# Optimization experiments

Hardware: AMD Instinct MI355X
Metric: run time of the kernel (lower is better)

Reference implementation:

```python
import jax, jax.numpy as jnp
import numpy as np

TOD, DOW = 288, 7
INPUT_LEN, OUTPUT_LEN = 12, 12
N_NODES, R_PATCH, LAYERS = 883, 8, 3
D_IN, D_NODE, D_TOD, D_DOW = 64, 32, 32, 32
DIMS = D_IN + D_NODE + D_TOD + D_DOW  # 160
HID = 2 * DIMS
NEG = -1e9  # finite large-negative mask (avoids NaN on fully-masked rows)


def setup_inputs():
    key = jax.random.key(0)
    ks = jax.random.split(key, 16)
    B = 8
    x = jax.random.normal(ks[0], (B, INPUT_LEN, N_NODES, 1), jnp.float32)
    te = jax.random.randint(ks[1], (B, INPUT_LEN, N_NODES, 2), 0, 7, dtype=jnp.int32)
    s = 0.1
    return {
        "x": x,
        "te": te,
        "patch_emb": jax.random.normal(ks[2], (R_PATCH, D_NODE), jnp.float32) * s,
        "node_table": jax.random.normal(ks[3], (N_NODES, D_NODE), jnp.float32) * s,
        "tod_emb": jax.random.normal(ks[4], (TOD, D_TOD), jnp.float32) * s,
        "dow_emb": jax.random.normal(ks[5], (DOW, D_DOW), jnp.float32) * s,
        "conv_W": jax.random.normal(ks[6], (D_IN, 3, INPUT_LEN), jnp.float32) * s,
        "conv_b": jnp.zeros((D_IN,), jnp.float32),
        # 4 layernorms per layer: [iro1, iro2, ier1, ier2]
        "ln_scale": jnp.ones((LAYERS, 4, DIMS), jnp.float32),
        "ln_bias": jnp.zeros((LAYERS, 4, DIMS), jnp.float32),
        # attn: axis1 = [iro, ier]; axis2 = [q, k, v, out], weights stored [in, out]
        "attn_W": jax.random.normal(ks[7], (LAYERS, 2, 4, DIMS, DIMS), jnp.float32) * 0.05,
        "attn_b": jnp.zeros((LAYERS, 2, 4, DIMS), jnp.float32),
        "mlp_W1": jax.random.normal(ks[8], (LAYERS, 2, DIMS, HID), jnp.float32) * 0.05,
        "mlp_b1": jnp.zeros((LAYERS, 2, HID), jnp.float32),
        "mlp_W2": jax.random.normal(ks[9], (LAYERS, 2, HID, DIMS), jnp.float32) * 0.05,
        "mlp_b2": jnp.zeros((LAYERS, 2, DIMS), jnp.float32),
        "out_W": jax.random.normal(ks[10], (OUTPUT_LEN, DIMS), jnp.float32) * 0.05,
        "out_b": jnp.zeros((OUTPUT_LEN,), jnp.float32),
    }


def _layernorm(x, g, b):
    mu = jnp.mean(x, axis=-1, keepdims=True)
    var = jnp.mean(jnp.square(x - mu), axis=-1, keepdims=True)
    return (x - mu) / jnp.sqrt(var + 1e-5) * g + b


def _mha(x, W, b, key_mask):
    # single-head attention (num_heads=1 in PatchID); x: [..., S, D]
    q = x @ W[0] + b[0]
    k = x @ W[1] + b[1]
    v = x @ W[2] + b[2]
    score = jnp.einsum('...sd,...td->...st', q, k) / np.sqrt(x.shape[-1]).astype(np.float32)
    score = jnp.where(key_mask[..., None, :], score, NEG)
    w = jax.nn.softmax(score, axis=-1)
    o = jnp.einsum('...st,...td->...sd', w, v)
    return o @ W[3] + b[3]


def _forward(x, te, patch_emb, node_table, tod_emb, dow_emb, conv_W, conv_b,
             ln_scale, ln_bias, attn_W, attn_b, mlp_W1, mlp_b1, mlp_W2, mlp_b2,
             out_W, out_b):
    N, R = N_NODES, R_PATCH
    # ---- PatchClassifier (router) ----
    logits = node_table @ patch_emb.T                       # [N, R]
    probs = jax.nn.softmax(logits, axis=-1)
    patch_ids = jnp.argmax(probs, axis=-1)                  # [N]
    hard = jax.nn.one_hot(patch_ids, R, dtype=probs.dtype)
    probs_st = hard - jax.lax.stop_gradient(probs) + probs  # straight-through
    node_soft = probs @ patch_emb                           # [N, D_NODE]
    # ---- embedding ----
    B, T_in = x.shape[0], x.shape[1]
    T = T_in // INPUT_LEN  # = 1
    tef = te.astype(x.dtype)
    x1 = jnp.concatenate([x, tef[..., 0:1] / TOD, tef[..., 1:2] / DOW], axis=-1)  # [B,T_in,N,3]
    x1 = x1.reshape(B, T, INPUT_LEN, N, 3)
    feat = jnp.einsum('btlnc,dcl->btnd', x1, conv_W) + conv_b  # patchified conv
    tid = te[:, -T:, :, 0]
    diw = te[:, -T:, :, 1]
    emb = jnp.concatenate([
        feat, tod_emb[tid], dow_emb[diw],
        jnp.broadcast_to(node_soft, (B, T, N, D_NODE)),
    ], axis=-1)                                             # [B,T,N,DIMS]
    # ---- group_by_patch (static P = N upper bound, masked) ----
    onehot = patch_ids[:, None] == jnp.arange(R)[None, :]
    pos = jnp.cumsum(onehot.astype(jnp.int32), axis=0)[jnp.arange(N), patch_ids] - 1
    P = N
    pf = jnp.zeros((B, T, R, P, DIMS), emb.dtype).at[:, :, patch_ids, pos, :].set(emb)
    mask2d = jnp.zeros((R, P), bool).at[patch_ids, pos].set(True)
    km_iro = mask2d[None, None]       # [1,1,R,P] valid-key mask, keys = P axis
    km_ier = mask2d.T[None, None]     # [1,1,P,R] valid-key mask, keys = R axis
    # ---- encoder layers ----
    for l in range(LAYERS):
        # intra-patch attention over P
        xn = _layernorm(pf, ln_scale[l, 0], ln_bias[l, 0])
        pf = pf + _mha(xn, attn_W[l, 0], attn_b[l, 0], km_iro)
        h = _layernorm(pf, ln_scale[l, 1], ln_bias[l, 1])
        pf = pf + (jax.nn.gelu(h @ mlp_W1[l, 0] + mlp_b1[l, 0], approximate=False)
                   @ mlp_W2[l, 0] + mlp_b2[l, 0])
        # inter-patch attention over R
        xt = jnp.swapaxes(pf, 2, 3)  # [B,T,P,R,D]
        xn = _layernorm(xt, ln_scale[l, 2], ln_bias[l, 2])
        xt = xt + _mha(xn, attn_W[l, 1], attn_b[l, 1], km_ier)
        pf = jnp.swapaxes(xt, 2, 3)
        h = _layernorm(pf, ln_scale[l, 3], ln_bias[l, 3])
        pf = pf + (jax.nn.gelu(h @ mlp_W1[l, 1] + mlp_b1[l, 1], approximate=False)
                   @ mlp_W2[l, 1] + mlp_b2[l, 1])
    # ---- ungroup + 1x1 output conv ----
    out_feat = pf[:, :, patch_ids, pos, :]                  # [B,T,N,DIMS]
    pred = jnp.einsum('btnd,od->bont', out_feat, out_W) + out_b[None, :, None, None]
    return pred, probs_st


def reference(x, te, patch_emb, node_table, tod_emb, dow_emb, conv_W, conv_b,
              ln_scale, ln_bias, attn_W, attn_b, mlp_W1, mlp_b1, mlp_W2, mlp_b2,
              out_W, out_b):
    return _forward(x, te, patch_emb, node_table, tod_emb, dow_emb, conv_W, conv_b,
                    ln_scale, ln_bias, attn_W, attn_b, mlp_W1, mlp_b1, mlp_W2,
                    mlp_b2, out_W, out_b)
```

## Files before the change

kernel.cpp:

```cpp
#include <hip/hip_runtime.h>
#include <math.h>

#define NNODES 883
#define BB 8
#define DIMS_ 160
#define HID_ 320
#define PBB 1008
#define RMAX2 (BB*PBB)
#define RMAXP (RMAX2+64)
#define GXNUM (RMAX2/16)

typedef __attribute__((ext_vector_type(8))) short short8v;
typedef __attribute__((ext_vector_type(4))) float fx4;
typedef __attribute__((ext_vector_type(4))) unsigned short ushort4v;

__device__ __forceinline__ unsigned short f2bf(float f) {
  unsigned int u = __float_as_uint(f);
  u = (u + 0x7fffu + ((u >> 16) & 1u)) >> 16;
  return (unsigned short)u;
}
__device__ __forceinline__ float bf2f(unsigned short u) {
  return __uint_as_float(((unsigned int)u) << 16);
}
__device__ __forceinline__ float gelu_f(float v) {
  return 0.5f*v*(1.f + erff(v*0.70710678118654752f));
}

__global__ __launch_bounds__(256)
void zero_pf(float4* __restrict__ p, int n4) {
  int i = blockIdx.x*256 + threadIdx.x;
  if (i < n4) p[i] = float4{0.f, 0.f, 0.f, 0.f};
}

__global__ __launch_bounds__(128)
void patch_kernel(const float* __restrict__ node_table,
                  const float* __restrict__ patch_emb,
                  float* __restrict__ probs_st,
                  float* __restrict__ nsoft,
                  int* __restrict__ patch_ids) {
  int n = blockIdx.x * blockDim.x + threadIdx.x;
  if (n >= NNODES) return;
  float nt[32];
#pragma unroll
  for (int j = 0; j < 32; ++j) nt[j] = node_table[n*32 + j];
  float lg[8];
#pragma unroll
  for (int r = 0; r < 8; ++r) {
    float a = 0.f;
#pragma unroll
    for (int j = 0; j < 32; ++j) a += nt[j] * patch_emb[r*32 + j];
    lg[r] = a;
  }
  float m = lg[0];
#pragma unroll
  for (int r = 1; r < 8; ++r) m = fmaxf(m, lg[r]);
  float e[8]; float s = 0.f;
#pragma unroll
  for (int r = 0; r < 8; ++r) { e[r] = expf(lg[r] - m); s += e[r]; }
  float p[8];
#pragma unroll
  for (int r = 0; r < 8; ++r) p[r] = e[r] / s;
  int am = 0; float best = p[0];
#pragma unroll
  for (int r = 1; r < 8; ++r) if (p[r] > best) { best = p[r]; am = r; }
  patch_ids[n] = am;
#pragma unroll
  for (int r = 0; r < 8; ++r) {
    float hard = (r == am) ? 1.f : 0.f;
    probs_st[n*8 + r] = (hard - p[r]) + p[r];
  }
#pragma unroll
  for (int j = 0; j < 32; ++j) {
    float a = 0.f;
#pragma unroll
    for (int r = 0; r < 8; ++r) a += p[r] * patch_emb[r*32 + j];
    nsoft[n*32 + j] = a;
  }
}

__global__ __launch_bounds__(1024)
void scan_kernel(const int* __restrict__ patch_ids,
                 int* __restrict__ pk, int* __restrict__ cnt,
                 int* __restrict__ offs, int* __restrict__ cntmax) {
  __shared__ int pid_s[NNODES];
  __shared__ int cnt_s[8], offs_s[8];
  int t = threadIdx.x;
  if (t < 8) cnt_s[t] = 0;
  for (int n = t; n < NNODES; n += 1024) pid_s[n] = patch_ids[n];
  __syncthreads();
  int p = -1, pos = 0;
  if (t < NNODES) {
    p = pid_s[t];
    atomicAdd(&cnt_s[p], 1);
    for (int m = 0; m < t; ++m) pos += (pid_s[m] == p) ? 1 : 0;
  }
  __syncthreads();
  if (t == 0) {
    int o = 0, mx = 0;
#pragma unroll
    for (int r = 0; r < 8; ++r) {
      offs_s[r] = o; offs[r] = o; cnt[r] = cnt_s[r];
      if (cnt_s[r] > mx) mx = cnt_s[r];
      o += (cnt_s[r] + 15) & ~15;
    }
    cntmax[0] = mx;
  }
  __syncthreads();
  if (t < NNODES) pk[t] = offs_s[p] + pos;
}

__global__ __launch_bounds__(160)
void embed_kernel(const float* __restrict__ x, const int* __restrict__ te,
                  const float* __restrict__ convW, const float* __restrict__ convB,
                  const float* __restrict__ tod, const float* __restrict__ dow,
                  const float* __restrict__ nsoft, const int* __restrict__ pk,
                  const float* __restrict__ g, const float* __restrict__ bt,
                  float* __restrict__ pf, unsigned short* __restrict__ xn) {
  int n = blockIdx.x, b = blockIdx.y, t = threadIdx.x;
  __shared__ float xs[3][12];
  __shared__ float rsum[160], rss[160];
  __shared__ float musv[2];
  if (t < 12) {
    int l = t;
    xs[0][l] = x[(b*12 + l)*NNODES + n];
    int base = ((b*12 + l)*NNODES + n)*2;
    xs[1][l] = (float)te[base]     / 288.0f;
    xs[2][l] = (float)te[base + 1] / 7.0f;
  }
  __syncthreads();
  int row = b*PBB + pk[n];
  float val;
  if (t < 64) {
    float a = convB[t];
#pragma unroll
    for (int c = 0; c < 3; ++c)
#pragma unroll
      for (int l = 0; l < 12; ++l)
        a += xs[c][l] * convW[t*36 + c*12 + l];
    val = a;
  } else if (t < 96) {
    int ti = te[((b*12 + 11)*NNODES + n)*2 + 0];
    val = tod[ti*32 + (t - 64)];
  } else if (t < 128) {
    int dw = te[((b*12 + 11)*NNODES + n)*2 + 1];
    val = dow[dw*32 + (t - 96)];
  } else {
    val = nsoft[n*32 + (t - 128)];
  }
  pf[row*DIMS_ + t] = val;
  rsum[t] = val; rss[t] = val*val;
  __syncthreads();
  if (t < 32) {
    float s = 0.f, ss = 0.f;
#pragma unroll
    for (int j = 0; j < 5; ++j) { s += rsum[t + 32*j]; ss += rss[t + 32*j]; }
    s  += __shfl_xor(s, 1, 32);  ss += __shfl_xor(ss, 1, 32);
    s  += __shfl_xor(s, 2, 32);  ss += __shfl_xor(ss, 2, 32);
    s  += __shfl_xor(s, 4, 32);  ss += __shfl_xor(ss, 4, 32);
    s  += __shfl_xor(s, 8, 32);  ss += __shfl_xor(ss, 8, 32);
    s  += __shfl_xor(s, 16, 32); ss += __shfl_xor(ss, 16, 32);
    if (t == 0) {
      float mu = s*(1.f/160.f);
      float var = ss*(1.f/160.f) - mu*mu;
      musv[0] = mu; musv[1] = rsqrtf(var + 1e-5f);
    }
  }
  __syncthreads();
  xn[(size_t)row*DIMS_ + t] = f2bf((val - musv[0])*musv[1]*g[t] + bt[t]);
}

__global__ __launch_bounds__(256)
void cvt_all(const float* __restrict__ attn_W, const float* __restrict__ mlp_W1,
             const float* __restrict__ mlp_W2,
             unsigned short* __restrict__ wt_attn, unsigned short* __restrict__ wt_w1,
             unsigned short* __restrict__ wt_w2) {
  int y = blockIdx.y;
  const float* src; unsigned short* dst; int K, N;
  if (y < 24)      { src = attn_W + (size_t)y*25600;        dst = wt_attn + (size_t)y*25600; K = 160; N = 160; }
  else if (y < 30) { int q = y-24; src = mlp_W1 + (size_t)q*160*320; dst = wt_w1 + (size_t)q*51200; K = 160; N = 320; }
  else             { int q = y-30; src = mlp_W2 + (size_t)q*320*160; dst = wt_w2 + (size_t)q*51200; K = 320; N = 160; }
  int tn = N >> 5, tk = K >> 5;
  int tile = blockIdx.x;
  if (tile >= tn*tk) return;
  int n0 = (tile % tn) << 5, k0 = (tile / tn) << 5;
  __shared__ unsigned short lds[32][33];
  int col = threadIdx.x & 31, rb = threadIdx.x >> 5;
#pragma unroll
  for (int rr = 0; rr < 4; ++rr) {
    int row = rb + 8*rr;
    lds[row][col] = f2bf(src[(size_t)(k0 + row)*N + n0 + col]);
  }
  __syncthreads();
#pragma unroll
  for (int rr = 0; rr < 4; ++rr) {
    int row = rb + 8*rr;
    dst[(size_t)(n0 + row)*K + k0 + col] = lds[col][row];
  }
}

template<int K, bool TRANSV, int CT>
__global__ __launch_bounds__(64)
void mfma_mm(const unsigned short* __restrict__ Xv, const unsigned short* __restrict__ Wt,
             const float* __restrict__ bias, unsigned short* __restrict__ Cv,
             int M, int Cstride, size_t Wystep, size_t Cystep, int bystep) {
  constexpr int NS = K / 32;
  int lane = threadIdx.x;
  int r15  = lane & 15;
  int kg   = lane >> 4;
  int row0 = blockIdx.x * 16;
  int colbase = blockIdx.y * (CT*16);
  int z = blockIdx.z;
  Wt   += (size_t)z * Wystep;
  bias += (size_t)z * bystep;

  int ar = row0 + r15; if (ar > M-1) ar = M-1;
  short8v afrag[NS];
  const unsigned short* Xr = Xv + (size_t)ar*K + kg*8;
#pragma unroll
  for (int t = 0; t < NS; ++t)
    afrag[t] = *(const short8v*)(const void*)(Xr + t*32);

  fx4 acc[CT];
#pragma unroll
  for (int n = 0; n < CT; ++n) acc[n] = (fx4){0.f,0.f,0.f,0.f};

  const unsigned short* Wb = Wt + (size_t)(colbase + r15)*K + kg*8;
#pragma unroll
  for (int t = 0; t < NS; ++t)
#pragma unroll
    for (int n = 0; n < CT; ++n) {
      short8v bfr = *(const short8v*)(const void*)(Wb + (size_t)n*16*K + t*32);
      acc[n] = __builtin_amdgcn_mfma_f32_16x16x32_bf16(afrag[t], bfr, acc[n], 0, 0, 0);
    }

  int orow0 = row0 + kg*4;
  unsigned short* C = Cv + (size_t)z * Cystep;
#pragma unroll
  for (int n = 0; n < CT; ++n) {
    int col = colbase + n*16 + r15;
    float bv = bias[col];
#pragma unroll
    for (int i = 0; i < 4; ++i) {
      int rr = orow0 + i;
      if (rr >= M) continue;
      unsigned short h = f2bf(acc[n][i] + bv);
      if (TRANSV && z == 2) C[(size_t)col*RMAXP + rr] = h;
      else                  C[(size_t)rr*Cstride + col] = h;
    }
  }
}

template<bool INTRA, bool HASNEXT, bool TRANSV_NEXT>
__global__ __launch_bounds__(512)
void fused_layer(const unsigned short* __restrict__ qb,
                 const unsigned short* __restrict__ kb,
                 const unsigned short* __restrict__ vt,
                 const unsigned short* __restrict__ wproj, const float* __restrict__ bproj,
                 const unsigned short* __restrict__ w1, const float* __restrict__ b1v,
                 const unsigned short* __restrict__ w2, const float* __restrict__ b2v,
                 const float* __restrict__ g1, const float* __restrict__ bt1,
                 const float* __restrict__ gn, const float* __restrict__ btn,
                 const unsigned short* __restrict__ wqkvN, const float* __restrict__ bqkvN,
                 float* __restrict__ pf, unsigned short* __restrict__ qbN, size_t CY,
                 const int* __restrict__ cnt, const int* __restrict__ offs) {
  __shared__ unsigned short L1s[16*192];
  __shared__ unsigned short L2s[16*320];
  __shared__ float sA[8][16], ssA[8][16];
  __shared__ float Sf[INTRA ? 16*256 : 1];
  __shared__ unsigned short Pl[INTRA ? 16*256 : 1];
  __shared__ float Sinv[16];
  __shared__ int cs[8], os[8];
  char* L1 = (char*)L1s; char* L2 = (char*)L2s; char* Pb = (char*)Pl;
  const float scale = 0.07905694150420949f;

  int tid = threadIdx.x;
  int wid = tid >> 6;
  int lane = tid & 63;
  int r15 = lane & 15, kg = lane >> 4;
  int row0 = blockIdx.x * 16;
  if (tid < 8) { cs[tid] = cnt[tid]; os[tid] = offs[tid]; }
  __syncthreads();
  int b = row0 / PBB;
  int local = row0 - b*PBB;
  int r = 7;
#pragma unroll
  for (int rr = 6; rr >= 0; --rr) if (local < os[rr+1]) r = rr;
  int L = cs[r];
  int q0 = local - os[r];
  int bo = b*PBB + os[r];
  int ntP = (wid < 2) ? 2 : 1;
  int ntM = (wid < 4) ? 3 : 2;

  if (INTRA) {
    int nkt = (L + 15) >> 4;
    int npv = (L + 31) >> 5;
    short8v qf[5];
    {
      const unsigned short* Qr = qb + (size_t)(row0 + r15)*DIMS_ + kg*8;
#pragma unroll
      for (int kk = 0; kk < 5; ++kk) qf[kk] = *(const short8v*)(const void*)(Qr + kk*32);
    }
#pragma unroll
    for (int u = 0; u < 2; ++u) {
      int t = wid + 8*u;
      if (t < nkt) {
        fx4 a = (fx4){0.f,0.f,0.f,0.f};
        const unsigned short* Kr = kb + (size_t)(bo + t*16 + r15)*DIMS_ + kg*8;
#pragma unroll
        for (int kk = 0; kk < 5; ++kk) {
          short8v kf = *(const short8v*)(const void*)(Kr + kk*32);
          a = __builtin_amdgcn_mfma_f32_16x16x32_bf16(qf[kk], kf, a, 0, 0, 0);
        }
        int j = t*16 + r15;
#pragma unroll
        for (int i = 0; i < 4; ++i)
          Sf[(4*kg + i)*256 + j] = (j < L) ? a[i]*scale : -1e30f;
// ... 247 lines not shown
#pragma unroll
  for (int u = 0; u < 2; ++u)
    if (u < ntP) {
      int n = wid + 8*u;
      int col = n*16 + r15;
      float bv = b2v[col];
#pragma unroll
      for (int i = 0; i < 4; ++i) {
        float v = pn[u][i] + acc3[u][i] + bv;
        fnv[u][i] = v;
        pf[(size_t)(row0 + 4*kg + i)*DIMS_ + col] = v;
        sv2[i] += v; ssv2[i] += v*v;
      }
    }
  if (!HASNEXT) return;

#pragma unroll
  for (int i = 0; i < 4; ++i) {
    sv2[i] += __shfl_xor(sv2[i], 1, 16); ssv2[i] += __shfl_xor(ssv2[i], 1, 16);
    sv2[i] += __shfl_xor(sv2[i], 2, 16); ssv2[i] += __shfl_xor(ssv2[i], 2, 16);
    sv2[i] += __shfl_xor(sv2[i], 4, 16); ssv2[i] += __shfl_xor(ssv2[i], 4, 16);
    sv2[i] += __shfl_xor(sv2[i], 8, 16); ssv2[i] += __shfl_xor(ssv2[i], 8, 16);
  }
  __syncthreads();
  if (r15 == 0) {
#pragma unroll
    for (int i = 0; i < 4; ++i) { sA[wid][4*kg+i] = sv2[i]; ssA[wid][4*kg+i] = ssv2[i]; }
  }
  __syncthreads();
#pragma unroll
  for (int i = 0; i < 4; ++i) {
    float st = 0.f, sst = 0.f;
#pragma unroll
    for (int w = 0; w < 8; ++w) { st += sA[w][4*kg+i]; sst += ssA[w][4*kg+i]; }
    mu[i] = st*(1.f/160.f);
    float var = sst*(1.f/160.f) - mu[i]*mu[i];
    rs[i] = rsqrtf(var + 1e-5f);
  }
#pragma unroll
  for (int u = 0; u < 2; ++u)
    if (u < ntP) {
      int n = wid + 8*u;
      int col = n*16 + r15;
      float gv = gn[col], bv = btn[col];
#pragma unroll
      for (int i = 0; i < 4; ++i) {
        int row = 4*kg + i;
        int byte = row*384 + ((col*2) ^ ((row & 7) << 4));
        *(unsigned short*)(L1 + byte) = f2bf((fnv[u][i] - mu[i])*rs[i]*gv + bv);
      }
    }
  __syncthreads();

  fx4 accq[4];
#pragma unroll
  for (int u = 0; u < 4; ++u) accq[u] = (fx4){0.f,0.f,0.f,0.f};
#pragma unroll
  for (int t = 0; t < 5; ++t) {
    short8v a4 = *(const short8v*)(const void*)(L1 + r15*384 + ((t*64 + kg*16) ^ ((r15 & 7) << 4)));
#pragma unroll
    for (int u = 0; u < 4; ++u) {
      int n = wid + 8*u;
      if (n < 30) {
        int z = n / 10, nn = n - z*10;
        short8v bfr = *(const short8v*)(const void*)
            (wqkvN + (size_t)z*25600 + (size_t)(nn*16 + r15)*160 + t*32 + kg*8);
        accq[u] = __builtin_amdgcn_mfma_f32_16x16x32_bf16(a4, bfr, accq[u], 0, 0, 0);
      }
    }
  }
#pragma unroll
  for (int u = 0; u < 4; ++u) {
    int n = wid + 8*u;
    if (n >= 30) continue;
    int z = n / 10, nn = n - z*10;
    int col = nn*16 + r15;
    float bv = bqkvN[z*160 + col];
    unsigned short* C = qbN + (size_t)z * CY;
#pragma unroll
    for (int i = 0; i < 4; ++i) {
      int rr = row0 + 4*kg + i;
      unsigned short h = f2bf(accq[u][i] + bv);
      if (TRANSV_NEXT && z == 2) C[(size_t)col*RMAXP + rr] = h;
      else                       C[(size_t)rr*DIMS_ + col] = h;
    }
  }
}

__global__ __launch_bounds__(256)
void out_kernel(const float* __restrict__ pf, const float* __restrict__ outW,
                const float* __restrict__ outB, const int* __restrict__ pk,
                float* __restrict__ out) {
  int idx = blockIdx.x*256 + threadIdx.x;
  if (idx >= BB*12*NNODES) return;
  int n = idx % NNODES;
  int rest = idx / NNODES;
  int o = rest % 12;
  int b = rest / 12;
  int row = b*PBB + pk[n];
  const float4* Pr = (const float4*)&pf[(size_t)row*DIMS_];
  const float4* Wr = (const float4*)&outW[o*DIMS_];
  float ax=0.f, ay=0.f, az=0.f, aw=0.f;
#pragma unroll
  for (int d4 = 0; d4 < 40; ++d4) {
    float4 a = Pr[d4], c = Wr[d4];
    ax += a.x*c.x; ay += a.y*c.y; az += a.z*c.z; aw += a.w*c.w;
  }
  out[idx] = (ax+ay+az+aw) + outB[o];
}

extern "C" void kernel_launch(void* const* d_in, const int* in_sizes, int n_in,
                              void* d_out, int out_size, void* d_ws, size_t ws_size,
                              hipStream_t stream) {
  const float* x         = (const float*)d_in[0];
  const int*   te        = (const int*)d_in[1];
  const float* patch_emb = (const float*)d_in[2];
  const float* node_tab  = (const float*)d_in[3];
  const float* tod_emb   = (const float*)d_in[4];
  const float* dow_emb   = (const float*)d_in[5];
  const float* conv_W    = (const float*)d_in[6];
  const float* conv_b    = (const float*)d_in[7];
  const float* ln_scale  = (const float*)d_in[8];
  const float* ln_bias   = (const float*)d_in[9];
  const float* attn_W    = (const float*)d_in[10];
  const float* attn_b    = (const float*)d_in[11];
  const float* mlp_W1    = (const float*)d_in[12];
  const float* mlp_b1    = (const float*)d_in[13];
  const float* mlp_W2    = (const float*)d_in[14];
  const float* mlp_b2    = (const float*)d_in[15];
  const float* out_W     = (const float*)d_in[16];
  const float* out_b     = (const float*)d_in[17];

  float* out = (float*)d_out;
  float* probs_st = out + BB*12*NNODES;

  const size_t CY = (size_t)(RMAX2 + 16) * DIMS_;

  char* W = (char*)d_ws;
  float* pf = (float*)W;                        W += (size_t)(RMAX2 + 16)*DIMS_*4;
  unsigned short* xn = (unsigned short*)W;      W += (size_t)(RMAX2 + 16)*DIMS_*2;
  unsigned short* qb = (unsigned short*)W;      W += CY*2;
  unsigned short* kb = (unsigned short*)W;      W += CY*2;
  unsigned short* vt = (unsigned short*)W;      W += (size_t)DIMS_*RMAXP*2;
  unsigned short* wt_attn = (unsigned short*)W; W += (size_t)24*160*160*2;
  unsigned short* wt_w1   = (unsigned short*)W; W += (size_t)6*320*160*2;
  unsigned short* wt_w2   = (unsigned short*)W; W += (size_t)6*160*320*2;
  float* nsoft = (float*)W;                     W += (size_t)NNODES*32*4;
  int* patch_ids = (int*)W;
  int* pk     = patch_ids + NNODES;
  int* cnt    = pk + NNODES;
  int* offs   = cnt + 8;
  int* cntmax = offs + 8;
  (void)vt;

  {
    int n4 = (RMAX2 + 16) * DIMS_ / 4;
    zero_pf<<<(n4 + 255)/256, 256, 0, stream>>>((float4*)pf, n4);
  }

  cvt_all<<<dim3(50, 36), 256, 0, stream>>>(attn_W, mlp_W1, mlp_W2, wt_attn, wt_w1, wt_w2);

  patch_kernel<<<(NNODES + 127)/128, 128, 0, stream>>>(node_tab, patch_emb, probs_st, nsoft, patch_ids);
  scan_kernel<<<1, 1024, 0, stream>>>(patch_ids, pk, cnt, offs, cntmax);
  embed_kernel<<<dim3(NNODES, BB), 160, 0, stream>>>(x, te, conv_W, conv_b, tod_emb, dow_emb,
                                                     nsoft, pk, ln_scale, ln_bias, pf, xn);

  mfma_mm<160,true,5><<<dim3(GXNUM,2,3), 64, 0, stream>>>(
      xn, wt_attn, attn_b, qb, RMAX2, DIMS_, 25600, CY, DIMS_);

  for (int l = 0; l < 3; ++l) {
    for (int a = 0; a < 2; ++a) {
      int wb = l*2 + a;
      const float* bbase = attn_b + (size_t)wb*4*DIMS_;
      const unsigned short* wqkv = wt_attn + (size_t)wb*4*25600;
      const float* g1  = ln_scale + (size_t)(l*4 + a*2 + 1)*DIMS_;
      const float* bt1 = ln_bias  + (size_t)(l*4 + a*2 + 1)*DIMS_;
      bool hasnext = !(l == 2 && a == 1);
      int nidx = (a == 0) ? (l*4 + 2) : ((l+1)*4);
      const float* gn  = hasnext ? ln_scale + (size_t)nidx*DIMS_ : nullptr;
      const float* btn = hasnext ? ln_bias  + (size_t)nidx*DIMS_ : nullptr;
      const unsigned short* wqkvN = hasnext ? wt_attn + (size_t)(wb+1)*4*25600 : nullptr;
      const float* bqkvN = hasnext ? attn_b + (size_t)(wb+1)*4*DIMS_ : nullptr;

      const unsigned short* wproj = wqkv + 3*25600;
      const float* bproj = bbase + 3*DIMS_;
      const unsigned short* w1 = wt_w1 + (size_t)wb*51200;
      const unsigned short* w2 = wt_w2 + (size_t)wb*51200;
      const float* b1v = mlp_b1 + (size_t)wb*HID_;
      const float* b2v = mlp_b2 + (size_t)wb*DIMS_;

      if (a == 0) {
        fused_layer<true,true,false><<<GXNUM, 512, 0, stream>>>(
            qb, qb + CY, qb + 2*CY, wproj, bproj, w1, b1v, w2, b2v,
            g1, bt1, gn, btn, wqkvN, bqkvN, pf, qb, CY, cnt, offs);
      } else if (hasnext) {
        fused_layer<false,true,true><<<GXNUM, 512, 0, stream>>>(
            qb, qb + CY, qb + 2*CY, wproj, bproj, w1, b1v, w2, b2v,
            g1, bt1, gn, btn, wqkvN, bqkvN, pf, qb, CY, cnt, offs);
      } else {
        fused_layer<false,false,false><<<GXNUM, 512, 0, stream>>>(
            qb, qb + CY, qb + 2*CY, wproj, bproj, w1, b1v, w2, b2v,
            g1, bt1, nullptr, nullptr, nullptr, nullptr, pf, qb, CY, cnt, offs);
      }
    }
  }

  out_kernel<<<(BB*12*NNODES + 255)/256, 256, 0, stream>>>(pf, out_W, out_b, pk, out);
}
```

Before: 276.8 us.

## Fuse all transformer layers into one cooperative kernel with grid syncs

```diff
diff --git a/kernel.cpp b/kernel.cpp
--- a/kernel.cpp
+++ b/kernel.cpp
@@ -1,5 +1,8 @@
 #include <hip/hip_runtime.h>
+#include <hip/hip_cooperative_groups.h>
 #include <math.h>
+
+namespace cg = cooperative_groups;
 
 #define NNODES 883
 #define BB 8
@@ -32,81 +35,75 @@
   if (i < n4) p[i] = float4{0.f, 0.f, 0.f, 0.f};
 }
 
-__global__ __launch_bounds__(128)
-void patch_kernel(const float* __restrict__ node_table,
-                  const float* __restrict__ patch_emb,
-                  float* __restrict__ probs_st,
-                  float* __restrict__ nsoft,
-                  int* __restrict__ patch_ids) {
-  int n = blockIdx.x * blockDim.x + threadIdx.x;
-  if (n >= NNODES) return;
-  float nt[32];
-#pragma unroll
-  for (int j = 0; j < 32; ++j) nt[j] = node_table[n*32 + j];
-  float lg[8];
-#pragma unroll
-  for (int r = 0; r < 8; ++r) {
-    float a = 0.f;
-#pragma unroll
-    for (int j = 0; j < 32; ++j) a += nt[j] * patch_emb[r*32 + j];
-    lg[r] = a;
-  }
-  float m = lg[0];
-#pragma unroll
-  for (int r = 1; r < 8; ++r) m = fmaxf(m, lg[r]);
-  float e[8]; float s = 0.f;
-#pragma unroll
-  for (int r = 0; r < 8; ++r) { e[r] = expf(lg[r] - m); s += e[r]; }
-  float p[8];
-#pragma unroll
-  for (int r = 0; r < 8; ++r) p[r] = e[r] / s;
-  int am = 0; float best = p[0];
-#pragma unroll
-  for (int r = 1; r < 8; ++r) if (p[r] > best) { best = p[r]; am = r; }
-  patch_ids[n] = am;
-#pragma unroll
-  for (int r = 0; r < 8; ++r) {
-    float hard = (r == am) ? 1.f : 0.f;
-    probs_st[n*8 + r] = (hard - p[r]) + p[r];
-  }
-#pragma unroll
-  for (int j = 0; j < 32; ++j) {
-    float a = 0.f;
-#pragma unroll
-    for (int r = 0; r < 8; ++r) a += p[r] * patch_emb[r*32 + j];
-    nsoft[n*32 + j] = a;
-  }
-}
-
 __global__ __launch_bounds__(1024)
-void scan_kernel(const int* __restrict__ patch_ids,
-                 int* __restrict__ pk, int* __restrict__ cnt,
-                 int* __restrict__ offs, int* __restrict__ cntmax) {
+void patch_scan(const float* __restrict__ node_table,
+                const float* __restrict__ patch_emb,
+                float* __restrict__ probs_st,
+                float* __restrict__ nsoft,
+                int* __restrict__ pk, int* __restrict__ cnt,
+                int* __restrict__ offs) {
+  __shared__ float pe[256];
   __shared__ int pid_s[NNODES];
   __shared__ int cnt_s[8], offs_s[8];
   int t = threadIdx.x;
+  for (int k = t; k < 256; k += 1024) pe[k] = patch_emb[k];
   if (t < 8) cnt_s[t] = 0;
-  for (int n = t; n < NNODES; n += 1024) pid_s[n] = patch_ids[n];
-  __syncthreads();
-  int p = -1, pos = 0;
+  __syncthreads();
+  int am = -1;
   if (t < NNODES) {
-    p = pid_s[t];
-    atomicAdd(&cnt_s[p], 1);
-    for (int m = 0; m < t; ++m) pos += (pid_s[m] == p) ? 1 : 0;
+    float nt[32];
+#pragma unroll
+    for (int j = 0; j < 32; ++j) nt[j] = node_table[t*32 + j];
+    float lg[8];
+#pragma unroll
+    for (int r = 0; r < 8; ++r) {
+      float a = 0.f;
+#pragma unroll
+      for (int j = 0; j < 32; ++j) a += nt[j] * pe[r*32 + j];
+      lg[r] = a;
+    }
+    float m = lg[0];
+#pragma unroll
+    for (int r = 1; r < 8; ++r) m = fmaxf(m, lg[r]);
+    float e[8]; float s = 0.f;
+#pragma unroll
+    for (int r = 0; r < 8; ++r) { e[r] = expf(lg[r] - m); s += e[r]; }
+    float p[8];
+#pragma unroll
+    for (int r = 0; r < 8; ++r) p[r] = e[r] / s;
+    am = 0; float best = p[0];
+#pragma unroll
+    for (int r = 1; r < 8; ++r) if (p[r] > best) { best = p[r]; am = r; }
+    pid_s[t] = am;
+    atomicAdd(&cnt_s[am], 1);
+#pragma unroll
+    for (int r = 0; r < 8; ++r) {
+      float hard = (r == am) ? 1.f : 0.f;
+      probs_st[t*8 + r] = (hard - p[r]) + p[r];
+    }
+#pragma unroll
+    for (int j = 0; j < 32; ++j) {
+      float a = 0.f;
+#pragma unroll
+      for (int r = 0; r < 8; ++r) a += p[r] * pe[r*32 + j];
+      nsoft[t*32 + j] = a;
+    }
   }
   __syncthreads();
   if (t == 0) {
-    int o = 0, mx = 0;
+    int o = 0;
 #pragma unroll
     for (int r = 0; r < 8; ++r) {
       offs_s[r] = o; offs[r] = o; cnt[r] = cnt_s[r];
-      if (cnt_s[r] > mx) mx = cnt_s[r];
       o += (cnt_s[r] + 15) & ~15;
     }
-    cntmax[0] = mx;
-  }
-  __syncthreads();
-  if (t < NNODES) pk[t] = offs_s[p] + pos;
+  }
+  __syncthreads();
+  if (t < NNODES) {
+    int pos = 0;
+    for (int m = 0; m < t; ++m) pos += (pid_s[m] == am) ? 1 : 0;
+    pk[t] = offs_s[am] + pos;
+  }
 }
 
 __global__ __launch_bounds__(160)
@@ -198,54 +195,446 @@
   }
 }
 
-template<int K, bool TRANSV, int CT>
-__global__ __launch_bounds__(64)
-void mfma_mm(const unsigned short* __restrict__ Xv, const unsigned short* __restrict__ Wt,
-             const float* __restrict__ bias, unsigned short* __restrict__ Cv,
-             int M, int Cstride, size_t Wystep, size_t Cystep, int bystep) {
-  constexpr int NS = K / 32;
-  int lane = threadIdx.x;
-  int r15  = lane & 15;
-  int kg   = lane >> 4;
+__device__ __forceinline__ void qkv_from_L1(const char* L1,
+    const unsigned short* __restrict__ wq, const float* __restrict__ bq,
+    unsigned short* __restrict__ qbN, bool transv,
+    int row0, int wid, int r15, int kg) {
+  constexpr size_t CY = (size_t)(RMAX2 + 16) * DIMS_;
+  fx4 accq[4];
+#pragma unroll
+  for (int u = 0; u < 4; ++u) accq[u] = (fx4){0.f,0.f,0.f,0.f};
+#pragma unroll
+  for (int t = 0; t < 5; ++t) {
+    short8v a4 = *(const short8v*)(const void*)(L1 + r15*384 + ((t*64 + kg*16) ^ ((r15 & 7) << 4)));
+#pragma unroll
+    for (int u = 0; u < 4; ++u) {
+      int n = wid + 8*u;
+      if (n < 30) {
+        int z = n / 10, nn = n - z*10;
+        short8v bfr = *(const short8v*)(const void*)
+            (wq + (size_t)z*25600 + (size_t)(nn*16 + r15)*160 + t*32 + kg*8);
+        accq[u] = __builtin_amdgcn_mfma_f32_16x16x32_bf16(a4, bfr, accq[u], 0, 0, 0);
+      }
+    }
+  }
+#pragma unroll
+  for (int u = 0; u < 4; ++u) {
+    int n = wid + 8*u;
+    if (n >= 30) continue;
+    int z = n / 10, nn = n - z*10;
+    int col = nn*16 + r15;
+    float bv = bq[z*160 + col];
+    unsigned short* C = qbN + (size_t)z * CY;
+#pragma unroll
+    for (int i = 0; i < 4; ++i) {
+      int rr = row0 + 4*kg + i;
+      unsigned short h = f2bf(accq[u][i] + bv);
+      if (transv && z == 2) C[(size_t)col*RMAXP + rr] = h;
+      else                  C[(size_t)rr*DIMS_ + col] = h;
+    }
+  }
+}
+
+__global__ __launch_bounds__(512, 4)
+void layers_coop(unsigned short* __restrict__ qbA, unsigned short* __restrict__ qbB,
+                 const unsigned short* __restrict__ wt_attn,
+                 const unsigned short* __restrict__ wt_w1,
+                 const unsigned short* __restrict__ wt_w2,
+                 const float* __restrict__ attn_b, const float* __restrict__ mlp_b1,
+                 const float* __restrict__ mlp_b2,
+                 const float* __restrict__ ln_scale, const float* __restrict__ ln_bias,
+                 const unsigned short* __restrict__ xn, float* __restrict__ pf,
+                 const int* __restrict__ cnt, const int* __restrict__ offs) {
+  constexpr size_t CY = (size_t)(RMAX2 + 16) * DIMS_;
+  cg::grid_group gg = cg::this_grid();
+  __shared__ unsigned short L1s[16*192];
+  __shared__ unsigned short L2s[16*320];
+  __shared__ float sA[8][16], ssA[8][16];
+  __shared__ float Sf[16*256];
+  __shared__ unsigned short Pl[16*256];
+  __shared__ float Sinv[16];
+  __shared__ int cs[8], os[8];
+  char* L1 = (char*)L1s; char* L2 = (char*)L2s; char* Pb = (char*)Pl;
+  const float scale = 0.07905694150420949f;
+
+  int tid = threadIdx.x;
+  int wid = tid >> 6;
+  int lane = tid & 63;
+  int r15 = lane & 15, kg = lane >> 4;
   int row0 = blockIdx.x * 16;
-  int colbase = blockIdx.y * (CT*16);
-  int z = blockIdx.z;
-  Wt   += (size_t)z * Wystep;
-  bias += (size_t)z * bystep;
-
-  int ar = row0 + r15; if (ar > M-1) ar = M-1;
-  short8v afrag[NS];
-  const unsigned short* Xr = Xv + (size_t)ar*K + kg*8;
-#pragma unroll
-  for (int t = 0; t < NS; ++t)
-    afrag[t] = *(const short8v*)(const void*)(Xr + t*32);
-
-  fx4 acc[CT];
-#pragma unroll
-  for (int n = 0; n < CT; ++n) acc[n] = (fx4){0.f,0.f,0.f,0.f};
-
-  const unsigned short* Wb = Wt + (size_t)(colbase + r15)*K + kg*8;
-#pragma unroll
-  for (int t = 0; t < NS; ++t)
-#pragma unroll
-    for (int n = 0; n < CT; ++n) {
-      short8v bfr = *(const short8v*)(const void*)(Wb + (size_t)n*16*K + t*32);
-      acc[n] = __builtin_amdgcn_mfma_f32_16x16x32_bf16(afrag[t], bfr, acc[n], 0, 0, 0);
-    }
-
-  int orow0 = row0 + kg*4;
-  unsigned short* C = Cv + (size_t)z * Cystep;
-#pragma unroll
-  for (int n = 0; n < CT; ++n) {
-    int col = colbase + n*16 + r15;
-    float bv = bias[col];
+  if (tid < 8) { cs[tid] = cnt[tid]; os[tid] = offs[tid]; }
+  __syncthreads();
+  int b = row0 / PBB;
+  int local = row0 - b*PBB;
+  int r = 7;
+#pragma unroll
+  for (int rr = 6; rr >= 0; --rr) if (local < os[rr+1]) r = rr;
+  int L = cs[r];
+  int q0 = local - os[r];
+  int bo = b*PBB + os[r];
+  int ntP = (wid < 2) ? 2 : 1;
+  int ntM = (wid < 4) ? 3 : 2;
+
+  for (int k = tid; k < 16*DIMS_; k += 512) {
+    int row = k / DIMS_, col = k - row*DIMS_;
+    int byte = row*384 + ((col*2) ^ ((row & 7) << 4));
+    *(unsigned short*)(L1 + byte) = xn[(size_t)(row0 + row)*DIMS_ + col];
+  }
+  __syncthreads();
+  qkv_from_L1(L1, wt_attn, attn_b, qbA, true, row0, wid, r15, kg);
+  __threadfence();
+  gg.sync();
+
+  for (int wb = 0; wb < 6; ++wb) {
+    bool intra = ((wb & 1) == 0);
+    bool hasnext = (wb < 5);
+    unsigned short* qbCur = (wb & 1) ? qbB : qbA;
+    unsigned short* qbNext = (wb & 1) ? qbA : qbB;
+    const unsigned short* qb = qbCur;
+    const unsigned short* kb = qbCur + CY;
+    const unsigned short* vt = qbCur + 2*CY;
+    const unsigned short* wqkv = wt_attn + (size_t)wb*4*25600;
+    const float* bbase = attn_b + (size_t)wb*4*DIMS_;
+    const unsigned short* wproj = wqkv + 3*25600;
+    const float* bproj = bbase + 3*DIMS_;
+    const unsigned short* w1 = wt_w1 + (size_t)wb*51200;
+    const unsigned short* w2 = wt_w2 + (size_t)wb*51200;
+    const float* b1v = mlp_b1 + (size_t)wb*HID_;
+    const float* b2v = mlp_b2 + (size_t)wb*DIMS_;
+    const float* g1  = ln_scale + (size_t)(2*wb + 1)*DIMS_;
+    const float* bt1 = ln_bias  + (size_t)(2*wb + 1)*DIMS_;
+    const float* gn  = ln_scale + (size_t)(2*wb + 2)*DIMS_;
+    const float* btn = ln_bias  + (size_t)(2*wb + 2)*DIMS_;
+    const unsigned short* wqkvN = wt_attn + (size_t)(wb+1)*4*25600;
+    const float* bqkvN = attn_b + (size_t)(wb+1)*4*DIMS_;
+
+    if (intra) {
+      int nkt = (L + 15) >> 4;
+      int npv = (L + 31) >> 5;
+      short8v qf[5];
+      {
+        const unsigned short* Qr = qb + (size_t)(row0 + r15)*DIMS_ + kg*8;
+#pragma unroll
+        for (int kk = 0; kk < 5; ++kk) qf[kk] = *(const short8v*)(const void*)(Qr + kk*32);
+      }
+#pragma unroll
+      for (int u = 0; u < 2; ++u) {
+        int t = wid + 8*u;
+        if (t < nkt) {
+          fx4 a = (fx4){0.f,0.f,0.f,0.f};
+          const unsigned short* Kr = kb + (size_t)(bo + t*16 + r15)*DIMS_ + kg*8;
+#pragma unroll
+          for (int kk = 0; kk < 5; ++kk) {
+            short8v kf = *(const short8v*)(const void*)(Kr + kk*32);
+            a = __builtin_amdgcn_mfma_f32_16x16x32_bf16(qf[kk], kf, a, 0, 0, 0);
+          }
+          int j = t*16 + r15;
+#pragma unroll
+          for (int i = 0; i < 4; ++i)
+            Sf[(4*kg + i)*256 + j] = (j < L) ? a[i]*scale : -1e30f;
+        }
+      }
+      __syncthreads();
+      {
+        int qq = lane >> 5, l32 = lane & 31;
+        int row = 2*wid + qq;
+        float vals[8];
+        float mx = -1e30f;
+#pragma unroll
+        for (int k = 0; k < 8; ++k) {
+          int j = l32 + 32*k;
+          float v = (j < L) ? Sf[row*256 + j] : -1e30f;
+          vals[k] = v; mx = fmaxf(mx, v);
+        }
+        mx = fmaxf(mx, __shfl_xor(mx, 1, 32));
+        mx = fmaxf(mx, __shfl_xor(mx, 2, 32));
+        mx = fmaxf(mx, __shfl_xor(mx, 4, 32));
+        mx = fmaxf(mx, __shfl_xor(mx, 8, 32));
+        mx = fmaxf(mx, __shfl_xor(mx, 16, 32));
+        float sum = 0.f;
+#pragma unroll
+        for (int k = 0; k < 8; ++k) {
+          float e = (vals[k] > -1e29f) ? expf(vals[k] - mx) : 0.f;
+          vals[k] = e; sum += e;
+        }
+        sum += __shfl_xor(sum, 1, 32);
+        sum += __shfl_xor(sum, 2, 32);
+        sum += __shfl_xor(sum, 4, 32);
+        sum += __shfl_xor(sum, 8, 32);
+        sum += __shfl_xor(sum, 16, 32);
+        if (l32 == 0) Sinv[row] = (sum > 0.f) ? 1.f/sum : 0.f;
+#pragma unroll
+        for (int k = 0; k < 8; ++k) {
+          int j = l32 + 32*k;
+          int byte = row*512 + ((j*2) ^ ((row & 7) << 4));
+          *(unsigned short*)(Pb + byte) = f2bf(vals[k]);
+        }
+      }
+      __syncthreads();
+      fx4 o[2];
+#pragma unroll
+      for (int u = 0; u < 2; ++u) o[u] = (fx4){0.f,0.f,0.f,0.f};
+#pragma unroll
+      for (int sS = 0; sS < 8; ++sS) {
+        if (sS < npv) {
+          short8v pfr = *(const short8v*)(const void*)
+              (Pb + r15*512 + ((sS*64 + kg*16) ^ ((r15 & 7) << 4)));
+#pragma unroll
+          for (int u = 0; u < 2; ++u)
+            if (u < ntP) {
+              int n = wid + 8*u;
+              const unsigned short* Vr = vt + (size_t)(n*16 + r15)*RMAXP + bo + sS*32 + kg*8;
+              short8v vf = *(const short8v*)(const void*)Vr;
+              o[u] = __builtin_amdgcn_mfma_f32_16x16x32_bf16(pfr, vf, o[u], 0, 0, 0);
+            }
+        }
+      }
+      float inv[4];
+#pragma unroll
+      for (int i = 0; i < 4; ++i) inv[i] = Sinv[4*kg + i];
+#pragma unroll
+      for (int u = 0; u < 2; ++u)
+        if (u < ntP) {
+          int n = wid + 8*u;
+#pragma unroll
+          for (int i = 0; i < 4; ++i) {
+            int row = 4*kg + i, d = n*16 + r15;
+            int byte = row*384 + ((d*2) ^ ((row & 7) << 4));
+            *(unsigned short*)(L1 + byte) = f2bf(o[u][i]*inv[i]);
+          }
+        }
+    } else {
+      int qq = lane >> 5, l32 = lane & 31;
+      int rowT = 2*wid + qq;
+      int p = q0 + rowT;
+      bool vq = p < L;
+      int j = l32 >> 2, c = l32 & 3;
+      int cj = cs[j];
+      bool vk = p < cj;
+      int keyrow = b*PBB + os[j] + (vk ? p : 0);
+      int qrow = row0 + rowT;
+      float part = 0.f;
+      {
+        const unsigned short* qr = qb + (size_t)qrow*DIMS_ + c*40;
+        const unsigned short* kr = kb + (size_t)keyrow*DIMS_ + c*40;
+#pragma unroll
+        for (int dd = 0; dd < 5; ++dd) {
+          short8v a8 = *(const short8v*)(const void*)(qr + dd*8);
+          short8v b8 = *(const short8v*)(const void*)(kr + dd*8);
+#pragma unroll
+          for (int u = 0; u < 8; ++u)
+            part += bf2f((unsigned short)a8[u]) * bf2f((unsigned short)b8[u]);
+        }
+      }
+      part += __shfl_xor(part, 1, 4);
+      part += __shfl_xor(part, 2, 4);
+      float sc = (vq && vk) ? part*scale : -1e30f;
+      float m = sc;
+      m = fmaxf(m, __shfl_xor(m, 4, 32));
+      m = fmaxf(m, __shfl_xor(m, 8, 32));
+      m = fmaxf(m, __shfl_xor(m, 16, 32));
+      float e = (vq && vk) ? expf(sc - m) : 0.f;
+      float sum = e;
+      sum += __shfl_xor(sum, 4, 32);
+      sum += __shfl_xor(sum, 8, 32);
+      sum += __shfl_xor(sum, 16, 32);
+      float w = (vq && vk && sum > 0.f) ? e/sum : 0.f;
+      float o[5];
+#pragma unroll
+      for (int k = 0; k < 5; ++k) o[k] = 0.f;
+      int qbase = qq*32;
+#pragma unroll
+      for (int jj = 0; jj < 8; ++jj) {
+        float wv = __shfl(w, qbase + jj*4);
+        int kr2 = __shfl(keyrow, qbase + jj*4);
+        if (wv > 0.f) {
+          const unsigned short* Vr = vt + (size_t)kr2*DIMS_;
+#pragma unroll
+          for (int k = 0; k < 5; ++k) o[k] += wv * bf2f(Vr[l32 + 32*k]);
+        }
+      }
+#pragma unroll
+      for (int k = 0; k < 5; ++k) {
+        int d = l32 + 32*k;
+        int byte = rowT*384 + ((d*2) ^ ((rowT & 7) << 4));
+        *(unsigned short*)(L1 + byte) = f2bf(vq ? o[k] : 0.f);
+      }
+    }
+    __syncthreads();
+
+    short8v af[5];
+#pragma unroll
+    for (int t = 0; t < 5; ++t)
+      af[t] = *(const short8v*)(const void*)(L1 + r15*384 + ((t*64 + kg*16) ^ ((r15 & 7) << 4)));
+    fx4 acc[2];
+#pragma unroll
+    for (int u = 0; u < 2; ++u) acc[u] = (fx4){0.f,0.f,0.f,0.f};
+#pragma unroll
+    for (int t = 0; t < 5; ++t)
+#pragma unroll
+      for (int u = 0; u < 2; ++u)
+        if (u < ntP) {
+          int n = wid + 8*u;
+          short8v bfr = *(const short8v*)(const void*)(wproj + (size_t)(n*16 + r15)*160 + t*32 + kg*8);
+          acc[u] = __builtin_amdgcn_mfma_f32_16x16x32_bf16(af[t], bfr, acc[u], 0, 0, 0);
+        }
+
+    float pn[2][4];
+    float sv[4] = {0,0,0,0}, ssv[4] = {0,0,0,0};
+#pragma unroll
+    for (int u = 0; u < 2; ++u)
+      if (u < ntP) {
+        int n = wid + 8*u;
+        int col = n*16 + r15;
+        float bv = bproj[col];
+#pragma unroll
+        for (int i = 0; i < 4; ++i) {
+          int row = row0 + 4*kg + i;
+          float v = pf[(size_t)row*DIMS_ + col] + acc[u][i] + bv;
+          pn[u][i] = v;
+          pf[(size_t)row*DIMS_ + col] = v;
+          sv[i] += v; ssv[i] += v*v;
+        }
+      }
 #pragma unroll
     for (int i = 0; i < 4; ++i) {
-      int rr = orow0 + i;
-      if (rr >= M) continue;
-      unsigned short h = f2bf(acc[n][i] + bv);
-      if (TRANSV && z == 2) C[(size_t)col*RMAXP + rr] = h;
-      else                  C[(size_t)rr*Cstride + col] = h;
+      sv[i] += __shfl_xor(sv[i], 1, 16); ssv[i] += __shfl_xor(ssv[i], 1, 16);
+      sv[i] += __shfl_xor(sv[i], 2, 16); ssv[i] += __shfl_xor(ssv[i], 2, 16);
+      sv[i] += __shfl_xor(sv[i], 4, 16); ssv[i] += __shfl_xor(ssv[i], 4, 16);
+      sv[i] += __shfl_xor(sv[i], 8, 16); ssv[i] += __shfl_xor(ssv[i], 8, 16);
+    }
+    if (r15 == 0) {
+#pragma unroll
+      for (int i = 0; i < 4; ++i) { sA[wid][4*kg+i] = sv[i]; ssA[wid][4*kg+i] = ssv[i]; }
+    }
+    __syncthreads();
+    float mu[4], rs[4];
+#pragma unroll
+    for (int i = 0; i < 4; ++i) {
+      float st = 0.f, sst = 0.f;
+#pragma unroll
+      for (int w = 0; w < 8; ++w) { st += sA[w][4*kg+i]; sst += ssA[w][4*kg+i]; }
+      mu[i] = st*(1.f/160.f);
+      float var = sst*(1.f/160.f) - mu[i]*mu[i];
+      rs[i] = rsqrtf(var + 1e-5f);
+    }
+#pragma unroll
+    for (int u = 0; u < 2; ++u)
+      if (u < ntP) {
+        int n = wid + 8*u;
+        int col = n*16 + r15;
+        float gv = g1[col], bv = bt1[col];
+#pragma unroll
+        for (int i = 0; i < 4; ++i) {
+          int row = 4*kg + i;
+          int byte = row*384 + ((col*2) ^ ((row & 7) << 4));
+          *(unsigned short*)(L1 + byte) = f2bf((pn[u][i] - mu[i])*rs[i]*gv + bv);
+        }
+      }
+    __syncthreads();
+
+    fx4 acc2[3];
+#pragma unroll
+    for (int u = 0; u < 3; ++u) acc2[u] = (fx4){0.f,0.f,0.f,0.f};
+#pragma unroll
+    for (int t = 0; t < 5; ++t) {
+      short8v a2 = *(const short8v*)(const void*)(L1 + r15*384 + ((t*64 + kg*16) ^ ((r15 & 7) << 4)));
+#pragma unroll
+      for (int u = 0; u < 3; ++u)
+        if (u < ntM) {
+          int n = wid + 8*u;
+          short8v bfr = *(const short8v*)(const void*)(w1 + (size_t)(n*16 + r15)*160 + t*32 + kg*8);
+          acc2[u] = __builtin_amdgcn_mfma_f32_16x16x32_bf16(a2, bfr, acc2[u], 0, 0, 0);
+        }
+    }
+#pragma unroll
+    for (int u = 0; u < 3; ++u)
+      if (u < ntM) {
+        int n = wid + 8*u;
+        int col = n*16 + r15;
+        float bv = b1v[col];
+#pragma unroll
+        for (int i = 0; i < 4; ++i) {
+          float v = gelu_f(acc2[u][i] + bv);
+          int row = 4*kg + i;
+          int byte = row*640 + ((col*2) ^ ((row & 7) << 4));
+          *(unsigned short*)(L2 + byte) = f2bf(v);
+        }
+      }
+    __syncthreads();
+
+    fx4 acc3[2];
+#pragma unroll
+    for (int u = 0; u < 2; ++u) acc3[u] = (fx4){0.f,0.f,0.f,0.f};
+#pragma unroll
+    for (int t = 0; t < 10; ++t) {
+      short8v a3 = *(const short8v*)(const void*)(L2 + r15*640 + ((t*64 + kg*16) ^ ((r15 & 7) << 4)));
+#pragma unroll
+      for (int u = 0; u < 2; ++u)
+        if (u < ntP) {
+          int n = wid + 8*u;
+          short8v bfr = *(const short8v*)(const void*)(w2 + (size_t)(n*16 + r15)*320 + t*32 + kg*8);
+          acc3[u] = __builtin_amdgcn_mfma_f32_16x16x32_bf16(a3, bfr, acc3[u], 0, 0, 0);
+        }
+    }
+    float sv2[4] = {0,0,0,0}, ssv2[4] = {0,0,0,0};
+    float fnv[2][4];
+#pragma unroll
+    for (int u = 0; u < 2; ++u)
+      if (u < ntP) {
+        int n = wid + 8*u;
+        int col = n*16 + r15;
+        float bv = b2v[col];
+#pragma unroll
+        for (int i = 0; i < 4; ++i) {
+          float v = pn[u][i] + acc3[u][i] + bv;
+          fnv[u][i] = v;
+          pf[(size_t)(row0 + 4*kg + i)*DIMS_ + col] = v;
+          sv2[i] += v; ssv2[i] += v*v;
+        }
+      }
+
+    if (hasnext) {
+#pragma unroll
+      for (int i = 0; i < 4; ++i) {
+        sv2[i] += __shfl_xor(sv2[i], 1, 16); ssv2[i] += __shfl_xor(ssv2[i], 1, 16);
+        sv2[i] += __shfl_xor(sv2[i], 2, 16); ssv2[i] += __shfl_xor(ssv2[i], 2, 16);
+        sv2[i] += __shfl_xor(sv2[i], 4, 16); ssv2[i] += __shfl_xor(ssv2[i], 4, 16);
+        sv2[i] += __shfl_xor(sv2[i], 8, 16); ssv2[i] += __shfl_xor(ssv2[i], 8, 16);
+      }
+      __syncthreads();
+      if (r15 == 0) {
+#pragma unroll
+        for (int i = 0; i < 4; ++i) { sA[wid][4*kg+i] = sv2[i]; ssA[wid][4*kg+i] = ssv2[i]; }
+      }
+      __syncthreads();
+#pragma unroll
+      for (int i = 0; i < 4; ++i) {
+        float st = 0.f, sst = 0.f;
+#pragma unroll
+        for (int w = 0; w < 8; ++w) { st += sA[w][4*kg+i]; sst += ssA[w][4*kg+i]; }
+        mu[i] = st*(1.f/160.f);
+        float var = sst*(1.f/160.f) - mu[i]*mu[i];
+        rs[i] = rsqrtf(var + 1e-5f);
+      }
+#pragma unroll
+      for (int u = 0; u < 2; ++u)
+        if (u < ntP) {
+          int n = wid + 8*u;
+          int col = n*16 + r15;
+          float gv = gn[col], bv = btn[col];
+#pragma unroll
+          for (int i = 0; i < 4; ++i) {
+            int row = 4*kg + i;
+            int byte = row*384 + ((col*2) ^ ((row & 7) << 4));
+            *(unsigned short*)(L1 + byte) = f2bf((fnv[u][i] - mu[i])*rs[i]*gv + bv);
+          }
+        }
+      __syncthreads();
+
+      qkv_from_L1(L1, wqkvN, bqkvN, qbNext, (wb & 1) != 0, row0, wid, r15, kg);
+      __threadfence();
+      gg.sync();
     }
   }
 }
@@ -261,7 +650,7 @@
                  const float* __restrict__ g1, const float* __restrict__ bt1,
                  const float* __restrict__ gn, const float* __restrict__ btn,
                  const unsigned short* __restrict__ wqkvN, const float* __restrict__ bqkvN,
-                 float* __restrict__ pf, unsigned short* __restrict__ qbN, size_t CY,
+                 float* __restrict__ pf, unsigned short* __restrict__ qbN,
                  const int* __restrict__ cnt, const int* __restrict__ offs) {
   __shared__ unsigned short L1s[16*192];
   __shared__ unsigned short L2s[16*320];
@@ -615,39 +1004,26 @@
     }
   __syncthreads();
 
-  fx4 accq[4];
-#pragma unroll
-  for (int u = 0; u < 4; ++u) accq[u] = (fx4){0.f,0.f,0.f,0.f};
-#pragma unroll
-  for (int t = 0; t < 5; ++t) {
-    short8v a4 = *(const short8v*)(const void*)(L1 + r15*384 + ((t*64 + kg*16) ^ ((r15 & 7) << 4)));
-#pragma unroll
-    for (int u = 0; u < 4; ++u) {
-      int n = wid + 8*u;
-      if (n < 30) {
-        int z = n / 10, nn = n - z*10;
-        short8v bfr = *(const short8v*)(const void*)
-            (wqkvN + (size_t)z*25600 + (size_t)(nn*16 + r15)*160 + t*32 + kg*8);
-        accq[u] = __builtin_amdgcn_mfma_f32_16x16x32_bf16(a4, bfr, accq[u], 0, 0, 0);
-      }
-    }
-  }
-#pragma unroll
-  for (int u = 0; u < 4; ++u) {
-    int n = wid + 8*u;
-    if (n >= 30) continue;
-    int z = n / 10, nn = n - z*10;
-    int col = nn*16 + r15;
-    float bv = bqkvN[z*160 + col];
-    unsigned short* C = qbN + (size_t)z * CY;
-#pragma unroll
-    for (int i = 0; i < 4; ++i) {
-      int rr = row0 + 4*kg + i;
-      unsigned short h = f2bf(accq[u][i] + bv);
-      if (TRANSV_NEXT && z == 2) C[(size_t)col*RMAXP + rr] = h;
-      else                       C[(size_t)rr*DIMS_ + col] = h;
-    }
-  }
+  qkv_from_L1(L1, wqkvN, bqkvN, qbN, TRANSV_NEXT, row0, wid, r15, kg);
+}
+
+__global__ __launch_bounds__(512)
+void qkv0_kernel(const unsigned short* __restrict__ xn,
+                 const unsigned short* __restrict__ wt_attn, const float* __restrict__ attn_b,
+                 unsigned short* __restrict__ qbA) {
+  __shared__ unsigned short L1s[16*192];
+  char* L1 = (char*)L1s;
+  int tid = threadIdx.x;
+  int wid = tid >> 6, lane = tid & 63;
+  int r15 = lane & 15, kg = lane >> 4;
+  int row0 = blockIdx.x * 16;
+  for (int k = tid; k < 16*DIMS_; k += 512) {
+    int row = k / DIMS_, col = k - row*DIMS_;
+    int byte = row*384 + ((col*2) ^ ((row & 7) << 4));
+    *(unsigned short*)(L1 + byte) = xn[(size_t)(row0 + row)*DIMS_ + col];
+  }
+  __syncthreads();
+  qkv_from_L1(L1, wt_attn, attn_b, qbA, true, row0, wid, r15, kg);
 }
 
 __global__ __launch_bounds__(256)
@@ -698,73 +1074,75 @@
   float* probs_st = out + BB*12*NNODES;
 
   const size_t CY = (size_t)(RMAX2 + 16) * DIMS_;
+  const size_t QBSZ = 2*CY + (size_t)DIMS_*RMAXP;
 
   char* W = (char*)d_ws;
   float* pf = (float*)W;                        W += (size_t)(RMAX2 + 16)*DIMS_*4;
   unsigned short* xn = (unsigned short*)W;      W += (size_t)(RMAX2 + 16)*DIMS_*2;
-  unsigned short* qb = (unsigned short*)W;      W += CY*2;
-  unsigned short* kb = (unsigned short*)W;      W += CY*2;
-  unsigned short* vt = (unsigned short*)W;      W += (size_t)DIMS_*RMAXP*2;
+  unsigned short* qbA = (unsigned short*)W;     W += QBSZ*2;
+  unsigned short* qbB = (unsigned short*)W;     W += QBSZ*2;
   unsigned short* wt_attn = (unsigned short*)W; W += (size_t)24*160*160*2;
   unsigned short* wt_w1   = (unsigned short*)W; W += (size_t)6*320*160*2;
   unsigned short* wt_w2   = (unsigned short*)W; W += (size_t)6*160*320*2;
   float* nsoft = (float*)W;                     W += (size_t)NNODES*32*4;
-  int* patch_ids = (int*)W;
-  int* pk     = patch_ids + NNODES;
-  int* cnt    = pk + NNODES;
-  int* offs   = cnt + 8;
-  int* cntmax = offs + 8;
-  (void)vt;
+  int* pk   = (int*)W;
+  int* cnt  = pk + NNODES;
+  int* offs = cnt + 8;
 
   {
     int n4 = (RMAX2 + 16) * DIMS_ / 4;
     zero_pf<<<(n4 + 255)/256, 256, 0, stream>>>((float4*)pf, n4);
   }
-
   cvt_all<<<dim3(50, 36), 256, 0, stream>>>(attn_W, mlp_W1, mlp_W2, wt_attn, wt_w1, wt_w2);
-
-  patch_kernel<<<(NNODES + 127)/128, 128, 0, stream>>>(node_tab, patch_emb, probs_st, nsoft, patch_ids);
-  scan_kernel<<<1, 1024, 0, stream>>>(patch_ids, pk, cnt, offs, cntmax);
+  patch_scan<<<1, 1024, 0, stream>>>(node_tab, patch_emb, probs_st, nsoft, pk, cnt, offs);
   embed_kernel<<<dim3(NNODES, BB), 160, 0, stream>>>(x, te, conv_W, conv_b, tod_emb, dow_emb,
                                                      nsoft, pk, ln_scale, ln_bias, pf, xn);
 
-  mfma_mm<160,true,5><<<dim3(GXNUM,2,3), 64, 0, stream>>>(
-      xn, wt_attn, attn_b, qb, RMAX2, DIMS_, 25600, CY, DIMS_);
-
-  for (int l = 0; l < 3; ++l) {
-    for (int a = 0; a < 2; ++a) {
-      int wb = l*2 + a;
+  int maxb = 0;
+  hipError_t occ = hipOccupancyMaxActiveBlocksPerMultiprocessor(&maxb, (const void*)layers_coop, 512, 0);
+  bool coop_ok = (occ == hipSuccess) && (maxb * 256 >= GXNUM);
+
+  if (coop_ok) {
+    void* args[] = {(void*)&qbA, (void*)&qbB, (void*)&wt_attn, (void*)&wt_w1, (void*)&wt_w2,
+                    (void*)&attn_b, (void*)&mlp_b1, (void*)&mlp_b2,
+                    (void*)&ln_scale, (void*)&ln_bias, (void*)&xn, (void*)&pf,
+                    (void*)&cnt, (void*)&offs};
+    hipError_t e = hipLaunchCooperativeKernel((const void*)layers_coop,
+                                              dim3(GXNUM), dim3(512), args, 0, stream);
+    coop_ok = (e == hipSuccess);
+  }
+
+  if (!coop_ok) {
+    qkv0_kernel<<<GXNUM, 512, 0, stream>>>(xn, wt_attn, attn_b, qbA);
+    for (int wb = 0; wb < 6; ++wb) {
+      unsigned short* qbCur = (wb & 1) ? qbB : qbA;
+      unsigned short* qbNext = (wb & 1) ? qbA : qbB;
+      const unsigned short* wqkv = wt_attn + (size_t)wb*4*25600;
       const float* bbase = attn_b + (size_t)wb*4*DIMS_;
-      const unsigned short* wqkv = wt_attn + (size_t)wb*4*25600;
-      const float* g1  = ln_scale + (size_t)(l*4 + a*2 + 1)*DIMS_;
-      const float* bt1 = ln_bias  + (size_t)(l*4 + a*2 + 1)*DIMS_;
-      bool hasnext = !(l == 2 && a == 1);
-      int nidx = (a == 0) ? (l*4 + 2) : ((l+1)*4);
-      const float* gn  = hasnext ? ln_scale + (size_t)nidx*DIMS_ : nullptr;
-      const float* btn = hasnext ? ln_bias  + (size_t)nidx*DIMS_ : nullptr;
-      const unsigned short* wqkvN = hasnext ? wt_attn + (size_t)(wb+1)*4*25600 : nullptr;
-      const float* bqkvN = hasnext ? attn_b + (size_t)(wb+1)*4*DIMS_ : nullptr;
-
       const unsigned short* wproj = wqkv + 3*25600;
       const float* bproj = bbase + 3*DIMS_;
       const unsigned short* w1 = wt_w1 + (size_t)wb*51200;
       const unsigned short* w2 = wt_w2 + (size_t)wb*51200;
       const float* b1v = mlp_b1 + (size_t)wb*HID_;
       const float* b2v = mlp_b2 + (size_t)wb*DIMS_;
-
-      if (a == 0) {
+      const float* g1  = ln_scale + (size_t)(2*wb + 1)*DIMS_;
+      const float* bt1 = ln_bias  + (size_t)(2*wb + 1)*DIMS_;
+      const float* gn  = ln_scale + (size_t)(2*wb + 2)*DIMS_;
+      const float* btn = ln_bias  + (size_t)(2*wb + 2)*DIMS_;
+      const unsigned short* wqkvN = wt_attn + (size_t)(wb+1)*4*25600;
+      const float* bqkvN = attn_b + (size_t)(wb+1)*4*DIMS_;
+      if (wb == 5)
+        fused_layer<false,false,false><<<GXNUM, 512, 0, stream>>>(
+            qbCur, qbCur + CY, qbCur + 2*CY, wproj, bproj, w1, b1v, w2, b2v,
+            g1, bt1, nullptr, nullptr, nullptr, nullptr, pf, qbNext, cnt, offs);
+      else if ((wb & 1) == 0)
         fused_layer<true,true,false><<<GXNUM, 512, 0, stream>>>(
-            qb, qb + CY, qb + 2*CY, wproj, bproj, w1, b1v, w2, b2v,
-            g1, bt1, gn, btn, wqkvN, bqkvN, pf, qb, CY, cnt, offs);
-      } else if (hasnext) {
+            qbCur, qbCur + CY, qbCur + 2*CY, wproj, bproj, w1, b1v, w2, b2v,
+            g1, bt1, gn, btn, wqkvN, bqkvN, pf, qbNext, cnt, offs);
+      else
         fused_layer<false,true,true><<<GXNUM, 512, 0, stream>>>(
-            qb, qb + CY, qb + 2*CY, wproj, bproj, w1, b1v, w2, b2v,
-            g1, bt1, gn, btn, wqkvN, bqkvN, pf, qb, CY, cnt, offs);
-      } else {
-        fused_layer<false,false,false><<<GXNUM, 512, 0, stream>>>(
-            qb, qb + CY, qb + 2*CY, wproj, bproj, w1, b1v, w2, b2v,
-            g1, bt1, nullptr, nullptr, nullptr, nullptr, pf, qb, CY, cnt, offs);
-      }
+            qbCur, qbCur + CY, qbCur + 2*CY, wproj, bproj, w1, b1v, w2, b2v,
+            g1, bt1, gn, btn, wqkvN, bqkvN, pf, qbNext, cnt, offs);
     }
   }
 
```

New measurement: 261.0 us. 5.7% less time.
